# Performance work log

Measured on AMD Instinct MI355X. Metric: run time of the kernel, lower is better.

Reference implementation:

```python
import jax, jax.numpy as jnp
import numpy as np

B = 256        # trees per batch
M = 1023       # nodes per tree (complete binary tree, depth 0..9)
N = B * M      # total flattened nodes
H = 128        # hidden dim
VOCAB = 100    # AST node-type vocab
NUM_CLASSES = 6
MAX_DEPTH = 10 # levels 0..9


def setup_inputs() -> dict:
    key = jax.random.key(0)
    k1, k2, k3, k4 = jax.random.split(key, 4)
    i = np.arange(M)
    parent_local = np.maximum((i - 1) // 2, 0)          # root points to itself
    depth_local = np.floor(np.log2(i + 1)).astype(np.int64)
    tree_off = np.arange(B, dtype=np.int64) * M
    parent_idx = (parent_local[None, :] + tree_off[:, None]).reshape(-1)
    depth = np.tile(depth_local, B)
    root_idx = tree_off
    return {
        "node_type": jax.random.randint(k1, (N,), 0, VOCAB, dtype=jnp.int64),
        "parent_idx": jnp.asarray(parent_idx),
        "depth": jnp.asarray(depth),
        "root_idx": jnp.asarray(root_idx),
        "E": jax.random.normal(k2, (VOCAB, H), dtype=jnp.float32) * 0.1,
        "Wh": jax.random.normal(k3, (H, H), dtype=jnp.float32) * (1.0 / np.sqrt(H)),
        "bh": jnp.zeros((H,), dtype=jnp.float32),
        "Wc": jax.random.normal(k4, (H, NUM_CLASSES), dtype=jnp.float32) * (1.0 / np.sqrt(H)),
        "bc": jnp.zeros((NUM_CLASSES,), dtype=jnp.float32),
    }


def reference(node_type, parent_idx, depth, root_idx, E, Wh, bh, Wc, bc):
    # Feature extraction: ast_class -> vector (Ast2VectorForPython analog)
    x = E[node_type]                         # [N, H]
    h = jnp.tanh(x)                          # leaves start from their own embedding
    # Leaf-to-root recursive propagation, one level at a time (children first).
    for d in range(MAX_DEPTH - 1, 0, -1):
        child_h = jnp.where((depth == d)[:, None], h, 0.0)
        agg = jax.ops.segment_sum(child_h, parent_idx, num_segments=N)  # [N, H]
        upd = jnp.tanh(x + agg @ Wh + bh)
        h = jnp.where((depth == d - 1)[:, None], upd, h)
    h_root = h[root_idx]                     # [B, H] == torch.stack(outputs, 0)
    logits = h_root @ Wc + bc                # nn.Linear(128, 6)
    return jax.nn.log_softmax(logits, axis=-1)
```

## Files before the change

### kernel.cpp

```cpp
#include <hip/hip_runtime.h>

#define TREES    256
#define MNODES   1023
#define HD       128
#define VOCAB_SZ 100
#define NCLS     6
#define NTHR     1024

typedef __attribute__((ext_vector_type(8))) short  short8;
typedef __attribute__((ext_vector_type(4))) unsigned short ushort4_t;
typedef __attribute__((ext_vector_type(4))) __bf16 bf16x4;
typedef __attribute__((ext_vector_type(8))) __bf16 bf16x8;
typedef __attribute__((ext_vector_type(4))) float  f32x4;

__device__ __forceinline__ unsigned short f2bf(float f) {
    unsigned int u = __float_as_uint(f);
    u += 0x7FFFu + ((u >> 16) & 1u);
    return (unsigned short)(u >> 16);
}
__device__ __forceinline__ float bf2f(unsigned short s) {
    return __uint_as_float(((unsigned int)s) << 16);
}
__device__ __forceinline__ float fast_tanh(float x) {
    float e = __expf(2.0f * x);
    return 1.0f - 2.0f / (e + 1.0f);
}

#define OFF_R1    0
#define OFF_R2    32768
#define OFF_ETBL  58368
#define OFF_NT    83968
#define OFF_BH    88064
#define OFF_HROOT 88576
#define LDS_BYTES 89088

template<int P, int MODE>
__device__ __forceinline__ void level_phase(
    unsigned char* lds, const unsigned char* bin, unsigned char* bout,
    const bf16x8 (&aT)[8], const float (&bhr)[8], const int* nt, int Loff,
    int cw, int l16, int lg, int g, float* hroot)
{
    constexpr int NBT = (P + 15) / 16;
    for (int bt = g; bt < NBT; bt += 4) {
        const int pb = bt * 16;
        const int p  = pb + l16;
        const int pc = (p < P) ? p : (P - 1);
        const int bswz = (pc & 7) << 4;
        bf16x8 bfrag[4];
#pragma unroll
        for (int kt = 0; kt < 4; ++kt)
            bfrag[kt] = __builtin_bit_cast(bf16x8,
                *(const short8*)(bin + pc * 256 + ((kt * 64 + lg * 16) ^ bswz)));
        f32x4 acc0 = {0.f, 0.f, 0.f, 0.f};
        f32x4 acc1 = {0.f, 0.f, 0.f, 0.f};
#pragma unroll
        for (int kt = 0; kt < 4; ++kt) {
            acc0 = __builtin_amdgcn_mfma_f32_16x16x32_bf16(aT[kt],     bfrag[kt], acc0, 0, 0, 0);
            acc1 = __builtin_amdgcn_mfma_f32_16x16x32_bf16(aT[4 + kt], bfrag[kt], acc1, 0, 0, 0);
        }
        const int ty   = nt[Loff + pc];
        const int tswz = (ty & 7) << 4;
        float h[8];
#pragma unroll
        for (int n2 = 0; n2 < 2; ++n2) {
            const int n0 = cw * 32 + n2 * 16 + lg * 4;
            const uint2 ev = *(const uint2*)(lds + OFF_ETBL + ty * 256 + ((n0 * 2) ^ tswz));
            const f32x4 a = n2 ? acc1 : acc0;
            h[n2*4+0] = fast_tanh(bf2f((unsigned short)(ev.x & 0xffffu)) + a[0] + bhr[n2*4+0]);
            h[n2*4+1] = fast_tanh(bf2f((unsigned short)(ev.x >> 16))     + a[1] + bhr[n2*4+1]);
            h[n2*4+2] = fast_tanh(bf2f((unsigned short)(ev.y & 0xffffu)) + a[2] + bhr[n2*4+2]);
            h[n2*4+3] = fast_tanh(bf2f((unsigned short)(ev.y >> 16))     + a[3] + bhr[n2*4+3]);
        }
        if (MODE == 1) {
            if (l16 == 0) {
#pragma unroll
                for (int n2 = 0; n2 < 2; ++n2) {
                    const int n0 = cw * 32 + n2 * 16 + lg * 4;
                    float4 v = {h[n2*4+0], h[n2*4+1], h[n2*4+2], h[n2*4+3]};
                    *(float4*)(hroot + n0) = v;
                }
            }
        } else {
#pragma unroll
            for (int u = 0; u < 8; ++u) h[u] += __shfl_xor(h[u], 1, 64);
            if ((p < P) && !(l16 & 1)) {
                const int orow = (pb >> 1) + (l16 >> 1);
                const int oswz = (orow & 7) << 4;
#pragma unroll
                for (int n2 = 0; n2 < 2; ++n2) {
                    const int n0 = cw * 32 + n2 * 16 + lg * 4;
                    bf16x4 pk = {(__bf16)h[n2*4+0], (__bf16)h[n2*4+1],
                                 (__bf16)h[n2*4+2], (__bf16)h[n2*4+3]};
                    *(bf16x4*)(bout + orow * 256 + ((n0 * 2) ^ oswz)) = pk;
                }
            }
        }
    }
}

__global__ __launch_bounds__(NTHR, 4)
void tree_rnn_kernel(const int* __restrict__ node_type,
                     const float* __restrict__ E,
                     const float* __restrict__ Wh,
                     const float* __restrict__ bh,
                     const float* __restrict__ Wc,
                     const float* __restrict__ bc,
                     float* __restrict__ out)
{
    __shared__ __align__(16) unsigned char lds[LDS_BYTES];
    int*   nt     = (int*)(lds + OFF_NT);
    float* bh_lds = (float*)(lds + OFF_BH);
    float* hroot  = (float*)(lds + OFF_HROOT);

    const int t    = blockIdx.x;
    const int tid  = threadIdx.x;
    const int lane = tid & 63;
    const int wv   = tid >> 6;
    const int l16  = lane & 15;
    const int lg   = lane >> 4;
    const int cw   = wv & 3;
    const int g    = wv >> 2;

    if (tid < MNODES) nt[tid] = node_type[t * MNODES + tid];
    if (tid < HD)     bh_lds[tid] = bh[tid];
    for (int i4 = tid; i4 < VOCAB_SZ * HD / 4; i4 += NTHR) {
        int row = i4 >> 5, c4 = i4 & 31;
        float4 v = ((const float4*)E)[i4];
        ushort4_t e, te;
        e[0] = f2bf(v.x); e[1] = f2bf(v.y); e[2] = f2bf(v.z); e[3] = f2bf(v.w);
        te[0] = f2bf(fast_tanh(v.x)); te[1] = f2bf(fast_tanh(v.y));
        te[2] = f2bf(fast_tanh(v.z)); te[3] = f2bf(fast_tanh(v.w));
        int boff = row * 256 + ((c4 * 8) ^ ((row & 7) << 4));
        *(ushort4_t*)(lds + OFF_ETBL + boff) = e;
        *(ushort4_t*)(lds + OFF_R1   + boff) = te;
    }

    bf16x8 aT[8];
    float  bhr[8];
#pragma unroll
    for (int n2 = 0; n2 < 2; ++n2) {
        const int col = cw * 32 + n2 * 16 + l16;
#pragma unroll
        for (int kt = 0; kt < 4; ++kt) {
            const int k0 = kt * 32 + lg * 8;
            short8 sv;
#pragma unroll
            for (int i = 0; i < 8; ++i) sv[i] = (short)f2bf(Wh[(k0 + i) * HD + col]);
            aT[n2 * 4 + kt] = __builtin_bit_cast(bf16x8, sv);
        }
        const int nb = cw * 32 + n2 * 16 + lg * 4;
#pragma unroll
        for (int r = 0; r < 4; ++r) bhr[n2 * 4 + r] = bh[nb + r];
    }
    __syncthreads();

    for (int bt = g; bt < 7; bt += 4) {
        const int tyr = bt * 16 + l16;
        const int tyc = (tyr < VOCAB_SZ) ? tyr : (VOCAB_SZ - 1);
        const int bswz = (tyc & 7) << 4;
        bf16x8 bfrag[4];
#pragma unroll
        for (int kt = 0; kt < 4; ++kt)
            bfrag[kt] = __builtin_bit_cast(bf16x8,
                *(const short8*)(lds + OFF_R1 + tyc * 256 + ((kt * 64 + lg * 16) ^ bswz)));
        f32x4 acc0 = {0.f, 0.f, 0.f, 0.f};
        f32x4 acc1 = {0.f, 0.f, 0.f, 0.f};
#pragma unroll
        for (int kt = 0; kt < 4; ++kt) {
            acc0 = __builtin_amdgcn_mfma_f32_16x16x32_bf16(aT[kt],     bfrag[kt], acc0, 0, 0, 0);
            acc1 = __builtin_amdgcn_mfma_f32_16x16x32_bf16(aT[4 + kt], bfrag[kt], acc1, 0, 0, 0);
        }
        if (tyr < VOCAB_SZ) {
            const int tswz = (tyr & 7) << 4;
#pragma unroll
            for (int n2 = 0; n2 < 2; ++n2) {
                const f32x4 a = n2 ? acc1 : acc0;
                const int n0 = cw * 32 + n2 * 16 + lg * 4;
                bf16x4 pk = {(__bf16)a[0], (__bf16)a[1], (__bf16)a[2], (__bf16)a[3]};
                *(bf16x4*)(lds + OFF_R2 + tyr * 256 + ((n0 * 2) ^ tswz)) = pk;
            }
        }
    }
    __syncthreads();

#pragma unroll
    for (int it = 0; it < 2; ++it) {
        int idx = it * NTHR + tid;
        int j   = idx >> 4;
        int c8  = idx & 15;
        int colb = c8 * 16;
        int tyP0 = nt[255 + 2 * j], tyP1 = nt[256 + 2 * j];
        int b9   = 511 + 4 * j;
        int tyAL = nt[b9], tyAR = nt[b9 + 1], tyBL = nt[b9 + 2], tyBR = nt[b9 + 3];
        short8 e0  = *(const short8*)(lds + OFF_ETBL + tyP0 * 256 + (colb ^ ((tyP0 & 7) << 4)));
        short8 e1  = *(const short8*)(lds + OFF_ETBL + tyP1 * 256 + (colb ^ ((tyP1 & 7) << 4)));
        short8 gAL = *(const short8*)(lds + OFF_R2   + tyAL * 256 + (colb ^ ((tyAL & 7) << 4)));
        short8 gAR = *(const short8*)(lds + OFF_R2   + tyAR * 256 + (colb ^ ((tyAR & 7) << 4)));
        short8 gBL = *(const short8*)(lds + OFF_R2   + tyBL * 256 + (colb ^ ((tyBL & 7) << 4)));
        short8 gBR = *(const short8*)(lds + OFF_R2   + tyBR * 256 + (colb ^ ((tyBR & 7) << 4)));
        float bhv[8];
        *(float4*)(bhv)     = *(const float4*)(bh_lds + c8 * 8);
        *(float4*)(bhv + 4) = *(const float4*)(bh_lds + c8 * 8 + 4);
        short8 o;
#pragma unroll
        for (int u = 0; u < 8; ++u) {
            float hA = fast_tanh(bf2f((unsigned short)e0[u]) + bf2f((unsigned short)gAL[u]) +
                                 bf2f((unsigned short)gAR[u]) + bhv[u]);
            float hB = fast_tanh(bf2f((unsigned short)e1[u]) + bf2f((unsigned short)gBL[u]) +
                                 bf2f((unsigned short)gBR[u]) + bhv[u]);
            o[u] = (short)f2bf(hA + hB);
        }
        *(short8*)(lds + OFF_R1 + j * 256 + (colb ^ ((j & 7) << 4))) = o;
    }
    __syncthreads();

    unsigned char* R1 = lds + OFF_R1;
    unsigned char* R2 = lds + OFF_R2;
    level_phase<128, 0>(lds, R1, R2, aT, bhr, nt, 127, cw, l16, lg, g, hroot); __syncthreads();
    level_phase< 64, 0>(lds, R2, R1, aT, bhr, nt,  63, cw, l16, lg, g, hroot); __syncthreads();
    level_phase< 32, 0>(lds, R1, R2, aT, bhr, nt,  31, cw, l16, lg, g, hroot); __syncthreads();
    level_phase< 16, 0>(lds, R2, R1, aT, bhr, nt,  15, cw, l16, lg, g, hroot); __syncthreads();
    level_phase<  8, 0>(lds, R1, R2, aT, bhr, nt,   7, cw, l16, lg, g, hroot); __syncthreads();
    level_phase<  4, 0>(lds, R2, R1, aT, bhr, nt,   3, cw, l16, lg, g, hroot); __syncthreads();
    level_phase<  2, 0>(lds, R1, R2, aT, bhr, nt,   1, cw, l16, lg, g, hroot); __syncthreads();
    level_phase<  1, 1>(lds, R2, R1, aT, bhr, nt,   0, cw, l16, lg, g, hroot); __syncthreads();

    if (tid < 64) {
        float hA = hroot[tid];
        float hB = hroot[tid + 64];
        float lgt[NCLS];
#pragma unroll
        for (int c = 0; c < NCLS; ++c) {
            float v = hA * Wc[tid * NCLS + c] + hB * Wc[(tid + 64) * NCLS + c];
#pragma unroll
            for (int off = 32; off > 0; off >>= 1)
                v += __shfl_xor(v, off, 64);
            lgt[c] = v + bc[c];
        }
        if (tid == 0) {
            float mx = lgt[0];
#pragma unroll
            for (int c = 1; c < NCLS; ++c) mx = fmaxf(mx, lgt[c]);
            float s = 0.f;
#pragma unroll
            for (int c = 0; c < NCLS; ++c) s += __expf(lgt[c] - mx);
            float lse = mx + __logf(s);
#pragma unroll
            for (int c = 0; c < NCLS; ++c) out[t * NCLS + c] = lgt[c] - lse;
        }
    }
}

extern "C" void kernel_launch(void* const* d_in, const int* in_sizes, int n_in,
                              void* d_out, int out_size, void* d_ws, size_t ws_size,
                              hipStream_t stream) {
    const int*   node_type = (const int*)d_in[0];
    const float* E  = (const float*)d_in[4];
    const float* Wh = (const float*)d_in[5];
    const float* bh = (const float*)d_in[6];
    const float* Wc = (const float*)d_in[7];
    const float* bc = (const float*)d_in[8];
    float* out = (float*)d_out;
    tree_rnn_kernel<<<dim3(TREES), dim3(NTHR), 0, stream>>>(node_type, E, Wh, bh, Wc, bc, out);
}
```

Baseline: 27.20 us.

## Split each tree into two subtree blocks plus a small root-combine kernel

```diff
diff --git a/kernel.cpp b/kernel.cpp
--- a/kernel.cpp
+++ b/kernel.cpp
@@ -13,10 +13,8 @@
 typedef __attribute__((ext_vector_type(8))) __bf16 bf16x8;
 typedef __attribute__((ext_vector_type(4))) float  f32x4;
 
-__device__ __forceinline__ unsigned short f2bf(float f) {
-    unsigned int u = __float_as_uint(f);
-    u += 0x7FFFu + ((u >> 16) & 1u);
-    return (unsigned short)(u >> 16);
+__device__ __forceinline__ unsigned short bfc(float f) {
+    return __builtin_bit_cast(unsigned short, (__bf16)f);
 }
 __device__ __forceinline__ float bf2f(unsigned short s) {
     return __uint_as_float(((unsigned int)s) << 16);
@@ -27,18 +25,16 @@
 }
 
 #define OFF_R1    0
-#define OFF_R2    32768
-#define OFF_ETBL  58368
-#define OFF_NT    83968
-#define OFF_BH    88064
-#define OFF_HROOT 88576
-#define LDS_BYTES 89088
+#define OFF_R2    25600
+#define OFF_ETBL  51200
+#define OFF_NT    76800
+#define LDS1      78848
 
 template<int P, int MODE>
 __device__ __forceinline__ void level_phase(
     unsigned char* lds, const unsigned char* bin, unsigned char* bout,
-    const bf16x8 (&aT)[8], const float (&bhr)[8], const int* nt, int Loff,
-    int cw, int l16, int lg, int g, float* hroot)
+    const bf16x8 (&aT)[8], const unsigned short* nt, int Loff,
+    int cw, int l16, int lg, int g, float* wsout)
 {
     constexpr int NBT = (P + 15) / 16;
     for (int bt = g; bt < NBT; bt += 4) {
@@ -66,10 +62,10 @@
             const int n0 = cw * 32 + n2 * 16 + lg * 4;
             const uint2 ev = *(const uint2*)(lds + OFF_ETBL + ty * 256 + ((n0 * 2) ^ tswz));
             const f32x4 a = n2 ? acc1 : acc0;
-            h[n2*4+0] = fast_tanh(bf2f((unsigned short)(ev.x & 0xffffu)) + a[0] + bhr[n2*4+0]);
-            h[n2*4+1] = fast_tanh(bf2f((unsigned short)(ev.x >> 16))     + a[1] + bhr[n2*4+1]);
-            h[n2*4+2] = fast_tanh(bf2f((unsigned short)(ev.y & 0xffffu)) + a[2] + bhr[n2*4+2]);
-            h[n2*4+3] = fast_tanh(bf2f((unsigned short)(ev.y >> 16))     + a[3] + bhr[n2*4+3]);
+            h[n2*4+0] = fast_tanh(bf2f((unsigned short)(ev.x & 0xffffu)) + a[0]);
+            h[n2*4+1] = fast_tanh(bf2f((unsigned short)(ev.x >> 16))     + a[1]);
+            h[n2*4+2] = fast_tanh(bf2f((unsigned short)(ev.y & 0xffffu)) + a[2]);
+            h[n2*4+3] = fast_tanh(bf2f((unsigned short)(ev.y >> 16))     + a[3]);
         }
         if (MODE == 1) {
             if (l16 == 0) {
@@ -77,7 +73,7 @@
                 for (int n2 = 0; n2 < 2; ++n2) {
                     const int n0 = cw * 32 + n2 * 16 + lg * 4;
                     float4 v = {h[n2*4+0], h[n2*4+1], h[n2*4+2], h[n2*4+3]};
-                    *(float4*)(hroot + n0) = v;
+                    *(float4*)(wsout + n0) = v;
                 }
             }
         } else {
@@ -98,21 +94,19 @@
     }
 }
 
-__global__ __launch_bounds__(NTHR, 4)
-void tree_rnn_kernel(const int* __restrict__ node_type,
-                     const float* __restrict__ E,
-                     const float* __restrict__ Wh,
-                     const float* __restrict__ bh,
-                     const float* __restrict__ Wc,
-                     const float* __restrict__ bc,
-                     float* __restrict__ out)
+__global__ __launch_bounds__(NTHR, 8)
+void k1_subtree(const int* __restrict__ node_type,
+                const float* __restrict__ E,
+                const float* __restrict__ Wh,
+                const float* __restrict__ bh,
+                float* __restrict__ ws)
 {
-    __shared__ __align__(16) unsigned char lds[LDS_BYTES];
-    int*   nt     = (int*)(lds + OFF_NT);
-    float* bh_lds = (float*)(lds + OFF_BH);
-    float* hroot  = (float*)(lds + OFF_HROOT);
-
-    const int t    = blockIdx.x;
+    __shared__ __align__(16) unsigned char lds[LDS1];
+    unsigned short* nt = (unsigned short*)(lds + OFF_NT);
+
+    const int b    = blockIdx.x;
+    const int t    = b >> 1;
+    const int s    = b & 1;
     const int tid  = threadIdx.x;
     const int lane = tid & 63;
     const int wv   = tid >> 6;
@@ -121,22 +115,22 @@
     const int cw   = wv & 3;
     const int g    = wv >> 2;
 
-    if (tid < MNODES) nt[tid] = node_type[t * MNODES + tid];
-    if (tid < HD)     bh_lds[tid] = bh[tid];
+    if (tid < MNODES) nt[tid] = (unsigned short)node_type[t * MNODES + tid];
     for (int i4 = tid; i4 < VOCAB_SZ * HD / 4; i4 += NTHR) {
         int row = i4 >> 5, c4 = i4 & 31;
-        float4 v = ((const float4*)E)[i4];
+        float4 v  = ((const float4*)E)[i4];
+        float4 bv = ((const float4*)bh)[c4];
         ushort4_t e, te;
-        e[0] = f2bf(v.x); e[1] = f2bf(v.y); e[2] = f2bf(v.z); e[3] = f2bf(v.w);
-        te[0] = f2bf(fast_tanh(v.x)); te[1] = f2bf(fast_tanh(v.y));
-        te[2] = f2bf(fast_tanh(v.z)); te[3] = f2bf(fast_tanh(v.w));
+        e[0] = bfc(v.x + bv.x); e[1] = bfc(v.y + bv.y);
+        e[2] = bfc(v.z + bv.z); e[3] = bfc(v.w + bv.w);
+        te[0] = bfc(fast_tanh(v.x)); te[1] = bfc(fast_tanh(v.y));
+        te[2] = bfc(fast_tanh(v.z)); te[3] = bfc(fast_tanh(v.w));
         int boff = row * 256 + ((c4 * 8) ^ ((row & 7) << 4));
         *(ushort4_t*)(lds + OFF_ETBL + boff) = e;
         *(ushort4_t*)(lds + OFF_R1   + boff) = te;
     }
 
     bf16x8 aT[8];
-    float  bhr[8];
 #pragma unroll
     for (int n2 = 0; n2 < 2; ++n2) {
         const int col = cw * 32 + n2 * 16 + l16;
@@ -145,12 +139,9 @@
             const int k0 = kt * 32 + lg * 8;
             short8 sv;
 #pragma unroll
-            for (int i = 0; i < 8; ++i) sv[i] = (short)f2bf(Wh[(k0 + i) * HD + col]);
+            for (int i = 0; i < 8; ++i) sv[i] = (short)bfc(Wh[(k0 + i) * HD + col]);
             aT[n2 * 4 + kt] = __builtin_bit_cast(bf16x8, sv);
         }
-        const int nb = cw * 32 + n2 * 16 + lg * 4;
-#pragma unroll
-        for (int r = 0; r < 4; ++r) bhr[n2 * 4 + r] = bh[nb + r];
     }
     __syncthreads();
 
@@ -183,32 +174,28 @@
     }
     __syncthreads();
 
-#pragma unroll
-    for (int it = 0; it < 2; ++it) {
-        int idx = it * NTHR + tid;
-        int j   = idx >> 4;
-        int c8  = idx & 15;
-        int colb = c8 * 16;
-        int tyP0 = nt[255 + 2 * j], tyP1 = nt[256 + 2 * j];
-        int b9   = 511 + 4 * j;
-        int tyAL = nt[b9], tyAR = nt[b9 + 1], tyBL = nt[b9 + 2], tyBR = nt[b9 + 3];
+    {
+        const int j   = tid >> 4;
+        const int c8  = tid & 15;
+        const int colb = c8 * 16;
+        const int o8  = 255 + s * 128 + 2 * j;
+        const int o9  = 511 + s * 256 + 4 * j;
+        int tyP0 = nt[o8], tyP1 = nt[o8 + 1];
+        int tyAL = nt[o9], tyAR = nt[o9 + 1], tyBL = nt[o9 + 2], tyBR = nt[o9 + 3];
         short8 e0  = *(const short8*)(lds + OFF_ETBL + tyP0 * 256 + (colb ^ ((tyP0 & 7) << 4)));
         short8 e1  = *(const short8*)(lds + OFF_ETBL + tyP1 * 256 + (colb ^ ((tyP1 & 7) << 4)));
         short8 gAL = *(const short8*)(lds + OFF_R2   + tyAL * 256 + (colb ^ ((tyAL & 7) << 4)));
         short8 gAR = *(const short8*)(lds + OFF_R2   + tyAR * 256 + (colb ^ ((tyAR & 7) << 4)));
         short8 gBL = *(const short8*)(lds + OFF_R2   + tyBL * 256 + (colb ^ ((tyBL & 7) << 4)));
         short8 gBR = *(const short8*)(lds + OFF_R2   + tyBR * 256 + (colb ^ ((tyBR & 7) << 4)));
-        float bhv[8];
-        *(float4*)(bhv)     = *(const float4*)(bh_lds + c8 * 8);
-        *(float4*)(bhv + 4) = *(const float4*)(bh_lds + c8 * 8 + 4);
         short8 o;
 #pragma unroll
         for (int u = 0; u < 8; ++u) {
             float hA = fast_tanh(bf2f((unsigned short)e0[u]) + bf2f((unsigned short)gAL[u]) +
-                                 bf2f((unsigned short)gAR[u]) + bhv[u]);
+                                 bf2f((unsigned short)gAR[u]));
             float hB = fast_tanh(bf2f((unsigned short)e1[u]) + bf2f((unsigned short)gBL[u]) +
-                                 bf2f((unsigned short)gBR[u]) + bhv[u]);
-            o[u] = (short)f2bf(hA + hB);
+                                 bf2f((unsigned short)gBR[u]));
+            o[u] = (short)bfc(hA + hB);
         }
         *(short8*)(lds + OFF_R1 + j * 256 + (colb ^ ((j & 7) << 4))) = o;
     }
@@ -216,38 +203,65 @@
 
     unsigned char* R1 = lds + OFF_R1;
     unsigned char* R2 = lds + OFF_R2;
-    level_phase<128, 0>(lds, R1, R2, aT, bhr, nt, 127, cw, l16, lg, g, hroot); __syncthreads();
-    level_phase< 64, 0>(lds, R2, R1, aT, bhr, nt,  63, cw, l16, lg, g, hroot); __syncthreads();
-    level_phase< 32, 0>(lds, R1, R2, aT, bhr, nt,  31, cw, l16, lg, g, hroot); __syncthreads();
-    level_phase< 16, 0>(lds, R2, R1, aT, bhr, nt,  15, cw, l16, lg, g, hroot); __syncthreads();
-    level_phase<  8, 0>(lds, R1, R2, aT, bhr, nt,   7, cw, l16, lg, g, hroot); __syncthreads();
-    level_phase<  4, 0>(lds, R2, R1, aT, bhr, nt,   3, cw, l16, lg, g, hroot); __syncthreads();
-    level_phase<  2, 0>(lds, R1, R2, aT, bhr, nt,   1, cw, l16, lg, g, hroot); __syncthreads();
-    level_phase<  1, 1>(lds, R2, R1, aT, bhr, nt,   0, cw, l16, lg, g, hroot); __syncthreads();
-
-    if (tid < 64) {
-        float hA = hroot[tid];
-        float hB = hroot[tid + 64];
-        float lgt[NCLS];
-#pragma unroll
-        for (int c = 0; c < NCLS; ++c) {
-            float v = hA * Wc[tid * NCLS + c] + hB * Wc[(tid + 64) * NCLS + c];
-#pragma unroll
-            for (int off = 32; off > 0; off >>= 1)
-                v += __shfl_xor(v, off, 64);
-            lgt[c] = v + bc[c];
-        }
-        if (tid == 0) {
-            float mx = lgt[0];
-#pragma unroll
-            for (int c = 1; c < NCLS; ++c) mx = fmaxf(mx, lgt[c]);
-            float s = 0.f;
-#pragma unroll
-            for (int c = 0; c < NCLS; ++c) s += __expf(lgt[c] - mx);
-            float lse = mx + __logf(s);
-#pragma unroll
-            for (int c = 0; c < NCLS; ++c) out[t * NCLS + c] = lgt[c] - lse;
-        }
+    float* wsout = ws + (t * 2 + s) * HD;
+    level_phase<64, 0>(lds, R1, R2, aT, nt, 127 + s * 64, cw, l16, lg, g, wsout); __syncthreads();
+    level_phase<32, 0>(lds, R2, R1, aT, nt,  63 + s * 32, cw, l16, lg, g, wsout); __syncthreads();
+    level_phase<16, 0>(lds, R1, R2, aT, nt,  31 + s * 16, cw, l16, lg, g, wsout); __syncthreads();
+    level_phase< 8, 0>(lds, R2, R1, aT, nt,  15 + s *  8, cw, l16, lg, g, wsout); __syncthreads();
+    level_phase< 4, 0>(lds, R1, R2, aT, nt,   7 + s *  4, cw, l16, lg, g, wsout); __syncthreads();
+    level_phase< 2, 0>(lds, R2, R1, aT, nt,   3 + s *  2, cw, l16, lg, g, wsout); __syncthreads();
+    level_phase< 1, 1>(lds, R1, R2, aT, nt,   1 + s,      cw, l16, lg, g, wsout);
+}
+
+__global__ __launch_bounds__(64)
+void k2_root(const int* __restrict__ node_type,
+             const float* __restrict__ E,
+             const float* __restrict__ Wh,
+             const float* __restrict__ bh,
+             const float* __restrict__ Wc,
+             const float* __restrict__ bc,
+             const float* __restrict__ ws,
+             float* __restrict__ out)
+{
+    __shared__ float agg[HD];
+    const int t    = blockIdx.x;
+    const int lane = threadIdx.x;
+
+    const float* w0 = ws + t * 2 * HD;
+    agg[lane]      = w0[lane]      + w0[HD + lane];
+    agg[lane + 64] = w0[lane + 64] + w0[HD + lane + 64];
+    __syncthreads();
+
+    float x0 = 0.f, x1 = 0.f;
+#pragma unroll 8
+    for (int k = 0; k < HD; ++k) {
+        float a = agg[k];
+        x0 += a * Wh[k * HD + lane];
+        x1 += a * Wh[k * HD + lane + 64];
+    }
+    int ty = node_type[t * MNODES];
+    float h0 = fast_tanh(E[ty * HD + lane]      + x0 + bh[lane]);
+    float h1 = fast_tanh(E[ty * HD + lane + 64] + x1 + bh[lane + 64]);
+
+    float lgt[NCLS];
+#pragma unroll
+    for (int c = 0; c < NCLS; ++c) {
+        float v = h0 * Wc[lane * NCLS + c] + h1 * Wc[(lane + 64) * NCLS + c];
+#pragma unroll
+        for (int off = 32; off > 0; off >>= 1)
+            v += __shfl_xor(v, off, 64);
+        lgt[c] = v + bc[c];
+    }
+    if (lane == 0) {
+        float mx = lgt[0];
+#pragma unroll
+        for (int c = 1; c < NCLS; ++c) mx = fmaxf(mx, lgt[c]);
+        float sum = 0.f;
+#pragma unroll
+        for (int c = 0; c < NCLS; ++c) sum += __expf(lgt[c] - mx);
+        float lse = mx + __logf(sum);
+#pragma unroll
+        for (int c = 0; c < NCLS; ++c) out[t * NCLS + c] = lgt[c] - lse;
     }
 }
 
@@ -261,5 +275,8 @@
     const float* Wc = (const float*)d_in[7];
     const float* bc = (const float*)d_in[8];
     float* out = (float*)d_out;
-    tree_rnn_kernel<<<dim3(TREES), dim3(NTHR), 0, stream>>>(node_type, E, Wh, bh, Wc, bc, out);
-}
+    float* ws  = (float*)d_ws;
+
+    k1_subtree<<<dim3(TREES * 2), dim3(NTHR), 0, stream>>>(node_type, E, Wh, bh, ws);
+    k2_root   <<<dim3(TREES),     dim3(64),   0, stream>>>(node_type, E, Wh, bh, Wc, bc, ws, out);
+}
```

Measured after the change: 44.60 us. 64.0% more time.
